# Kernel tuning notes

Hardware: AMD Instinct MI355X
Metric: run time of the kernel (lower is better)

Reference implementation:

```python
import jax, jax.numpy as jnp
import numpy as np

LEAKY = 0.2  # tf.nn.leaky_relu default alpha
E_SZ = [64, 64, 16]
F_SZ = [128, 128, 8]
N_MAPS, C, H, W = 64, 1, 32, 32
B = 8192


def _leaky(x):
    return jnp.where(x >= 0, x, LEAKY * x)


def func_theta(x, theta, sz, in_sz):
    # x: [B, in_sz]; theta: [B, total]; per-sample MLP with weights sliced from theta
    y = x
    offset = 0
    n = len(sz)
    for i, out_sz in enumerate(sz):
        w_sz = in_sz * out_sz
        Wm = theta[:, offset:offset + w_sz].reshape(-1, in_sz, out_sz)
        offset += w_sz
        b = theta[:, offset:offset + out_sz]
        offset += out_sz
        y = jnp.einsum('bi,bio->bo', y, Wm) + b
        if i < n - 1:
            y = _leaky(y)
        in_sz = out_sz
    return y


def setup_inputs() -> dict:
    key = jax.random.key(0)
    ks = jax.random.split(key, 16)

    def g(k, shape, scale):
        return (jax.random.normal(k, shape, dtype=jnp.float32) * scale)

    inp = {
        'indices': jax.random.randint(ks[0], (B,), 0, N_MAPS, dtype=jnp.int32),
        'states': jax.random.normal(ks[1], (B, 4), dtype=jnp.float32),
        'maps': jax.random.normal(ks[2], (N_MAPS, C, H, W), dtype=jnp.float32),
        'fc1_w': g(ks[3], (C * H * W, 256), 1.0 / np.sqrt(C * H * W)),
        'fc1_b': jnp.zeros((256,), jnp.float32),
        'fc2_w': g(ks[4], (256, 128), 1.0 / np.sqrt(256)),
        'fc2_b': jnp.zeros((128,), jnp.float32),
        'fc3_w': g(ks[5], (128, 128), 1.0 / np.sqrt(128)),
        'fc3_b': jnp.zeros((128,), jnp.float32),
        'bn_w': g(ks[6], (128, 32), 1.0 / np.sqrt(128)),
        'bn_b': jnp.zeros((32,), jnp.float32),
        'e_w': g(ks[7], (32, 5456), 1e-5),
        'e_b': g(ks[8], (5456,), 1e-3),
        'f_w': g(ks[9], (32, 21768), 1e-5),
        'f_b': g(ks[10], (21768,), 1e-3),
    }
    return inp


def reference(indices, states, maps, fc1_w, fc1_b, fc2_w, fc2_b, fc3_w, fc3_b,
              bn_w, bn_b, e_w, e_b, f_w, f_b):
    # gather maps per sample and flatten (NCHW -> NHWC transpose is a no-op after flatten
    # mathematically, but keep the exact data layout of the original)
    m = jnp.transpose(maps[indices], (0, 2, 3, 1)).astype(jnp.float32)  # [B,H,W,C]
    z = m.reshape(m.shape[0], -1)

    # hypernet trunk
    z = _leaky(z @ fc1_w + fc1_b)
    z = _leaky(z @ fc2_w + fc2_b)
    z = _leaky(z @ fc3_w + fc3_b)
    z = z @ bn_w + bn_b  # bottleneck, no activation
    theta_e = z @ e_w + e_b  # [B, 5456]
    theta_f = z @ f_w + f_b  # [B, 21768]

    S = states[:, 0:2]
    G = states[:, 2:4]
    e_s = func_theta(S, theta_e, E_SZ, 2)
    e_g = func_theta(G, theta_e, E_SZ, 2)
    zf = jnp.concatenate([e_s, e_g], axis=-1)  # [B, 32]
    ang = func_theta(zf, theta_f, F_SZ, 2 * E_SZ[-1])  # [B, 8]
    pts = jnp.concatenate([jnp.sin(ang), jnp.cos(ang)], axis=-1)  # [B, 16]
    return pts
```

## Files before the change

### kernel.cpp

```cpp
#include <hip/hip_runtime.h>
#include <hip/hip_bf16.h>


#define LEAKY 0.2f
#define NCLS 64
#define B_TOT 8192
#define NSLICE 4
#define ESTRIDE 68
#define FSTRIDE 132


__device__ __forceinline__ float lrelu(float x) { return x >= 0.f ? x : LEAKY * x; }

__global__ __launch_bounds__(1024) void backbone_bucket_kernel(
    const float* __restrict__ maps,
    const float* __restrict__ fc1_w, const float* __restrict__ fc1_b,
    const float* __restrict__ fc2_w, const float* __restrict__ fc2_b,
    const float* __restrict__ fc3_w, const float* __restrict__ fc3_b,
    const float* __restrict__ bn_w,  const float* __restrict__ bn_b,
    float* __restrict__ z,
    const int* __restrict__ idx, int* __restrict__ counts,
    int* __restrict__ offsets, int* __restrict__ perm)
{
    __shared__ float m[1024];
    __shared__ __align__(16) float4 red4[1024];
    __shared__ __align__(16) float h1[256];
    __shared__ __align__(16) float h2[128];
    __shared__ __align__(16) float h3[128];
    __shared__ int cnt[16][64];
    __shared__ int wcur[16][64];

    const int t = threadIdx.x;

    if (blockIdx.x == 64) {
        const int w = t >> 6;
        cnt[w][t & 63] = 0;
        __syncthreads();
        int my[8];
#pragma unroll
        for (int r = 0; r < 8; ++r) {
            my[r] = idx[r * 1024 + t];
            atomicAdd(&cnt[w][my[r]], 1);
        }
        __syncthreads();
        if (t < 64) {
            int run = 0;
#pragma unroll
            for (int w2 = 0; w2 < 16; ++w2) {
                const int v = cnt[w2][t];
                wcur[w2][t] = run;
                run += v;
            }
            counts[t] = run;
            int x = run;
            for (int d = 1; d < 64; d <<= 1) {
                const int y = __shfl_up(x, d, 64);
                if (t >= d) x += y;
            }
            const int basec = x - run;
            offsets[t] = basec;
#pragma unroll
            for (int w2 = 0; w2 < 16; ++w2) wcur[w2][t] += basec;
        }
        __syncthreads();
#pragma unroll
        for (int r = 0; r < 8; ++r) {
            const int p = atomicAdd(&wcur[w][my[r]], 1);
            perm[p] = r * 1024 + t;
        }
        return;
    }

    const int c = blockIdx.x;
    m[t] = maps[(size_t)c * 1024 + t];
    __syncthreads();

    {
        const int og = t & 63, ks = t >> 6;
        const float* wp = fc1_w + og * 4;
        float4 acc = {0.f, 0.f, 0.f, 0.f};
#pragma unroll 8
        for (int i = 0; i < 64; ++i) {
            const int k = ks * 64 + i;
            const float mk = m[k];
            const float4 w = *(const float4*)&wp[(size_t)k * 256];
            acc.x += mk * w.x; acc.y += mk * w.y;
            acc.z += mk * w.z; acc.w += mk * w.w;
        }
        red4[t] = acc;
    }
    __syncthreads();
    if (t < 64) {
        float4 a = *(const float4*)&fc1_b[t * 4];
#pragma unroll
        for (int r = 0; r < 16; ++r) {
            const float4 v = red4[r * 64 + t];
            a.x += v.x; a.y += v.y; a.z += v.z; a.w += v.w;
        }
        a.x = lrelu(a.x); a.y = lrelu(a.y); a.z = lrelu(a.z); a.w = lrelu(a.w);
        *(float4*)&h1[t * 4] = a;
    }
    __syncthreads();
    {
        const int og = t & 31, ks = t >> 5;
        float4 acc = {0.f, 0.f, 0.f, 0.f};
#pragma unroll
        for (int i = 0; i < 8; ++i) {
            const int k = ks * 8 + i;
            const float hk = h1[k];
            const float4 w = *(const float4*)&fc2_w[k * 128 + og * 4];
            acc.x += hk * w.x; acc.y += hk * w.y;
            acc.z += hk * w.z; acc.w += hk * w.w;
        }
        red4[t] = acc;
    }
    __syncthreads();
    if (t < 32) {
        float4 a = *(const float4*)&fc2_b[t * 4];
#pragma unroll
        for (int r = 0; r < 32; ++r) {
            const float4 v = red4[r * 32 + t];
            a.x += v.x; a.y += v.y; a.z += v.z; a.w += v.w;
        }
        a.x = lrelu(a.x); a.y = lrelu(a.y); a.z = lrelu(a.z); a.w = lrelu(a.w);
        *(float4*)&h2[t * 4] = a;
    }
    __syncthreads();
    {
        const int og = t & 31, ks = t >> 5;
        float4 acc = {0.f, 0.f, 0.f, 0.f};
#pragma unroll
        for (int i = 0; i < 4; ++i) {
            const int k = ks * 4 + i;
            const float hk = h2[k];
            const float4 w = *(const float4*)&fc3_w[k * 128 + og * 4];
            acc.x += hk * w.x; acc.y += hk * w.y;
            acc.z += hk * w.z; acc.w += hk * w.w;
        }
        red4[t] = acc;
    }
    __syncthreads();
    if (t < 32) {
        float4 a = *(const float4*)&fc3_b[t * 4];
#pragma unroll
        for (int r = 0; r < 32; ++r) {
            const float4 v = red4[r * 32 + t];
            a.x += v.x; a.y += v.y; a.z += v.z; a.w += v.w;
        }
        a.x = lrelu(a.x); a.y = lrelu(a.y); a.z = lrelu(a.z); a.w = lrelu(a.w);
        *(float4*)&h3[t * 4] = a;
    }
    __syncthreads();
    {
        const int og = t & 7, ks = t >> 3;
        const float hk = h3[ks];
        const float4 w = *(const float4*)&bn_w[ks * 32 + og * 4];
        float4 acc;
        acc.x = hk * w.x; acc.y = hk * w.y; acc.z = hk * w.z; acc.w = hk * w.w;
        red4[t] = acc;
    }
    __syncthreads();
    if (t < 8) {
        float4 a = *(const float4*)&bn_b[t * 4];
#pragma unroll
        for (int r = 0; r < 128; ++r) {
            const float4 v = red4[r * 8 + t];
            a.x += v.x; a.y += v.y; a.z += v.z; a.w += v.w;
        }
        *(float4*)&z[c * 32 + t * 4] = a;
    }
}

__global__ __launch_bounds__(256) void theta_kernel(
    const float* __restrict__ z,
    const float* __restrict__ e_w, const float* __restrict__ e_b,
    const float* __restrict__ f_w, const float* __restrict__ f_b,
    float* __restrict__ th_e, float* __restrict__ th_f)
{
    __shared__ __align__(16) float zl[2048];
    const int t = threadIdx.x;
    ((float4*)zl)[t]       = ((const float4*)z)[t];
    ((float4*)zl)[t + 256] = ((const float4*)z)[t + 256];
    __syncthreads();

    int j = blockIdx.x * 256 + t;
    const int cbase = blockIdx.y * 8;
    const float* wbase;
    float* op;
    int stride;
    float bias;
    if (j < 5456) {
        wbase = e_w + j; bias = e_b[j]; op = th_e + j; stride = 5456;
    } else {
        const int jj = j - 5456;
        if (jj >= 21768) return;
        wbase = f_w + jj; bias = f_b[jj]; op = th_f + jj; stride = 21768;
    }
    float wk[32];
#pragma unroll
    for (int k = 0; k < 32; ++k) wk[k] = wbase[(size_t)k * stride];

#pragma unroll
    for (int cc = 0; cc < 8; cc += 4) {
        const int c0 = cbase + cc;
        float a0 = bias, a1 = bias, a2 = bias, a3 = bias;
#pragma unroll
        for (int k4 = 0; k4 < 8; ++k4) {
            const float4 z0 = *(const float4*)&zl[(c0 + 0) * 32 + k4 * 4];
            const float4 z1 = *(const float4*)&zl[(c0 + 1) * 32 + k4 * 4];
            const float4 z2 = *(const float4*)&zl[(c0 + 2) * 32 + k4 * 4];
            const float4 z3 = *(const float4*)&zl[(c0 + 3) * 32 + k4 * 4];
            const float w0 = wk[k4 * 4], w1 = wk[k4 * 4 + 1];
            const float w2 = wk[k4 * 4 + 2], w3 = wk[k4 * 4 + 3];
            a0 += z0.x * w0 + z0.y * w1 + z0.z * w2 + z0.w * w3;
            a1 += z1.x * w0 + z1.y * w1 + z1.z * w2 + z1.w * w3;
            a2 += z2.x * w0 + z2.y * w1 + z2.z * w2 + z2.w * w3;
            a3 += z3.x * w0 + z3.y * w1 + z3.z * w2 + z3.w * w3;
        }
        op[(size_t)(c0 + 0) * stride] = a0;
        op[(size_t)(c0 + 1) * stride] = a1;
        op[(size_t)(c0 + 2) * stride] = a2;
        op[(size_t)(c0 + 3) * stride] = a3;
    }
}

__global__ __launch_bounds__(512) void func_kernel(
    const float* __restrict__ states,
    const float* __restrict__ th_e_all, const float* __restrict__ th_f_all,
    const int* __restrict__ counts, const int* __restrict__ offsets,
    const int* __restrict__ perm, float* __restrict__ out)
{
    __shared__ __align__(16) float wbuf[5392];
    __shared__ __align__(16) float w3fb[1160];
    __shared__ __align__(16) float actA[4352];
    __shared__ __align__(16) float actB[4352];
    __shared__ __align__(16) float part[512];

    const int c = blockIdx.x;
    const int s = blockIdx.y;
    const int nb   = counts[c];
    const int base = offsets[c];
    const int chunk = (nb + NSLICE - 1) / NSLICE;
    const int k0 = s * chunk;
    const int k1 = (nb < k0 + chunk) ? nb : (k0 + chunk);
    const int cnt = (k1 > k0) ? (k1 - k0) : 0;
    if (cnt == 0) return;

    const float* te = th_e_all + (size_t)c * 5456;
    const float* tf = th_f_all + (size_t)c * 21768;

    const int t   = threadIdx.x;
    const int vbs = t & 15;
    const int ce  = (t >> 4) * 2;
    const int fbs = t & 7;
    const int cf  = (t >> 3) * 2;

    for (int j = t * 4; j < 1160; j += 2048)
        *(float4*)&w3fb[j] = *(const float4*)&tf[20608 + j];
    for (int j = t * 4; j < 5392; j += 2048)
        *(float4*)&wbuf[j] = *(const float4*)&te[j];

    const int passes = (cnt + 31) >> 5;
    for (int p = 0; p < passes; ++p) {
        __syncthreads();
        if (p) {
            for (int j = t * 4; j < 5392; j += 2048)
                *(float4*)&wbuf[j] = *(const float4*)&te[j];
            __syncthreads();
        }

        const int kkA = k0 + p * 32 + vbs;
        const int kkB = kkA + 16;
        const int biA = (kkA < k1) ? perm[base + kkA] : 0;
        const int biB = (kkB < k1) ? perm[base + kkB] : 0;
        const float4 stA = *(const float4*)&states[(size_t)biA * 4];
        const float4 stB = *(const float4*)&states[(size_t)biB * 4];
        const float i0[4] = {stA.x, stB.x, stA.z, stB.z};
        const float i1[4] = {stA.y, stB.y, stA.w, stB.w};

        {
            const float2 wa = *(const float2*)&wbuf[ce];
            const float2 wb = *(const float2*)&wbuf[64 + ce];
            const float2 bb = *(const float2*)&wbuf[128 + ce];
#pragma unroll
            for (int j = 0; j < 4; ++j) {
                float2 o;
                o.x = lrelu(i0[j] * wa.x + i1[j] * wb.x + bb.x);
                o.y = lrelu(i0[j] * wa.y + i1[j] * wb.y + bb.y);
                *(float2*)&actA[(vbs + 16 * j) * ESTRIDE + ce] = o;
            }
        }
        __syncthreads();

        {
            float a0[4] = {0, 0, 0, 0}, a1[4] = {0, 0, 0, 0};
#pragma unroll 4
            for (int k4 = 0; k4 < 16; ++k4) {
                float4 y[4];
#pragma unroll
                for (int j = 0; j < 4; ++j)
                    y[j] = *(const float4*)&actA[(vbs + 16 * j) * ESTRIDE + k4 * 4];
#pragma unroll
                for (int u = 0; u < 4; ++u) {
                    const float2 w = *(const float2*)&wbuf[192 + (k4 * 4 + u) * 64 + ce];
#pragma unroll
                    for (int j = 0; j < 4; ++j) {
                        const float yv = (&y[j].x)[u];
                        a0[j] += yv * w.x;
                        a1[j] += yv * w.y;
                    }
                }
            }
            const float2 b2 = *(const float2*)&wbuf[4288 + ce];
#pragma unroll
            for (int j = 0; j < 4; ++j) {
                float2 o;
                o.x = lrelu(a0[j] + b2.x);
                o.y = lrelu(a1[j] + b2.y);
                *(float2*)&actB[(vbs + 16 * j) * ESTRIDE + ce] = o;
            }
        }
        __syncthreads();

        if (t < 256) {
            const int c3 = t >> 4;
            float a[4] = {0, 0, 0, 0};
#pragma unroll 4
            for (int k4 = 0; k4 < 16; ++k4) {
                float4 y[4];
#pragma unroll
                for (int j = 0; j < 4; ++j)
                    y[j] = *(const float4*)&actB[(vbs + 16 * j) * ESTRIDE + k4 * 4];
#pragma unroll
                for (int u = 0; u < 4; ++u) {
                    const float w = wbuf[4352 + (k4 * 4 + u) * 16 + c3];
#pragma unroll
                    for (int j = 0; j < 4; ++j) a[j] += (&y[j].x)[u] * w;
                }
            }
            const float b3 = wbuf[5376 + c3];
#pragma unroll
            for (int j = 0; j < 4; ++j) {
                const int vb = vbs + 16 * j;
                actA[(vb & 31) * FSTRIDE + (vb >> 5) * 16 + c3] = a[j] + b3;
            }
        }
        __syncthreads();

        for (int j = t * 4; j < 4224; j += 2048)
            *(float4*)&wbuf[j] = *(const float4*)&tf[j];
        __syncthreads();

        {
            float a0[4] = {0, 0, 0, 0}, a1[4] = {0, 0, 0, 0};
#pragma unroll
            for (int k4 = 0; k4 < 8; ++k4) {
                float4 y[4];
#pragma unroll
                for (int j = 0; j < 4; ++j)
                    y[j] = *(const float4*)&actA[(fbs + 8 * j) * FSTRIDE + k4 * 4];
#pragma unroll
                for (int u = 0; u < 4; ++u) {
                    const float2 w = *(const float2*)&wbuf[(k4 * 4 + u) * 128 + cf];
#pragma unroll
                    for (int j = 0; j < 4; ++j) {
                        const float yv = (&y[j].x)[u];
                        a0[j] += yv * w.x;
                        a1[j] += yv * w.y;
                    }
                }
            }
            const float2 b1 = *(const float2*)&wbuf[4096 + cf];
#pragma unroll
            for (int j = 0; j < 4; ++j) {
                float2 o;
                o.x = lrelu(a0[j] + b1.x);
                o.y = lrelu(a1[j] + b1.y);
                *(float2*)&actB[(fbs + 8 * j) * FSTRIDE + cf] = o;
            }
        }
        __syncthreads();

        {
            float a0[4] = {0, 0, 0, 0}, a1[4] = {0, 0, 0, 0};
#pragma unroll
            for (int h = 0; h < 4; ++h) {
                if (h) __syncthreads();
                for (int j = t * 4; j < 4096; j += 2048)
                    *(float4*)&wbuf[j] = *(const float4*)&tf[4224 + h * 4096 + j];
                __syncthreads();
#pragma unroll 4
                for (int k4 = 0; k4 < 8; ++k4) {
                    float4 y[4];
#pragma unroll
                    for (int j = 0; j < 4; ++j)
                        y[j] = *(const float4*)&actB[(fbs + 8 * j) * FSTRIDE + h * 32 + k4 * 4];
#pragma unroll
                    for (int u = 0; u < 4; ++u) {
                        const float2 w = *(const float2*)&wbuf[(k4 * 4 + u) * 128 + cf];
#pragma unroll
                        for (int j = 0; j < 4; ++j) {
                            const float yv = (&y[j].x)[u];
                            a0[j] += yv * w.x;
                            a1[j] += yv * w.y;
                        }
                    }
                }
            }
            const float2 b2 = *(const float2*)&w3fb[cf];
#pragma unroll
            for (int j = 0; j < 4; ++j) {
                float2 o;
                o.x = lrelu(a0[j] + b2.x);
                o.y = lrelu(a1[j] + b2.y);
                *(float2*)&actA[(fbs + 8 * j) * FSTRIDE + cf] = o;
            }
        }
        __syncthreads();

        {
            const int bat = t & 31, c8 = (t >> 5) & 7, kh = t >> 8;
            float a = 0.f;
#pragma unroll 4
            for (int k4 = kh * 16; k4 < kh * 16 + 16; ++k4) {
                const float4 y = *(const float4*)&actA[bat * FSTRIDE + k4 * 4];
#pragma unroll
                for (int u = 0; u < 4; ++u)
                    a += (&y.x)[u] * w3fb[128 + (k4 * 4 + u) * 8 + c8];
            }
            part[kh * 256 + bat * 8 + c8] = a;
        }
        __syncthreads();
        if (t < 256) {
            const int bat = t & 31, c8 = t >> 5;
            const int kk = k0 + p * 32 + bat;
            if (kk < k1) {
                const int bi = perm[base + kk];
                const float a = part[bat * 8 + c8] + part[256 + bat * 8 + c8]
                              + w3fb[1152 + c8];
                out[(size_t)bi * 16 + c8]     = __sinf(a);
                out[(size_t)bi * 16 + 8 + c8] = __cosf(a);
            }
        }
    }
}

extern "C" void kernel_launch(void* const* d_in, const int* in_sizes, int n_in,
                              void* d_out, int out_size, void* d_ws, size_t ws_size,
                              hipStream_t stream)
{
    const int*   indices = (const int*)  d_in[0];
    const float* states  = (const float*)d_in[1];
    const float* maps    = (const float*)d_in[2];
    const float* fc1_w   = (const float*)d_in[3];
    const float* fc1_b   = (const float*)d_in[4];
    const float* fc2_w   = (const float*)d_in[5];
    const float* fc2_b   = (const float*)d_in[6];
    const float* fc3_w   = (const float*)d_in[7];
    const float* fc3_b   = (const float*)d_in[8];
    const float* bn_w    = (const float*)d_in[9];
    const float* bn_b    = (const float*)d_in[10];
    const float* e_w     = (const float*)d_in[11];
    const float* e_b     = (const float*)d_in[12];
    const float* f_w     = (const float*)d_in[13];
    const float* f_b     = (const float*)d_in[14];
    float* out = (float*)d_out;

    float* ws   = (float*)d_ws;
    float* z    = ws;
    float* th_e = ws + 2048;
    float* th_f = ws + 351232;
    int* counts  = (int*)(ws + 1744384);
    int* offsets = counts + 64;
    int* perm    = counts + 128;

    backbone_bucket_kernel<<<65, 1024, 0, stream>>>(
        maps, fc1_w, fc1_b, fc2_w, fc2_b, fc3_w, fc3_b, bn_w, bn_b, z,
        indices, counts, offsets, perm);
    theta_kernel<<<dim3(107, 8), 256, 0, stream>>>(
        z, e_w, e_b, f_w, f_b, th_e, th_f);
    func_kernel<<<dim3(NCLS, NSLICE), 512, 0, stream>>>(
        states, th_e, th_f, counts, offsets, perm, out);
}
```

Measured before the change: 146.4 us.

## Halve per-pass batch, double slices, and prefetch theta weights into registers

The func kernel now processes 16 samples per pass instead of 32 and uses 8 slices per class instead of 4, so more blocks are launched. Each thread works on one sample with four output columns. Theta weight chunks are prefetched into registers one stage ahead, and stage-2 weights are loaded in two 8192-float halves rather than four, to overlap global loads with compute. Shared memory use drops and launch bounds request 4 blocks per CU for higher occupancy. The trade-off is more register pressure and redundant weight loads across the extra slices.

New measurement: 157.6 us. 7.7% more time.

```diff
diff --git a/kernel.cpp b/kernel.cpp
--- a/kernel.cpp
+++ b/kernel.cpp
@@ -5,9 +5,9 @@
 #define LEAKY 0.2f
 #define NCLS 64
 #define B_TOT 8192
-#define NSLICE 4
-#define ESTRIDE 68
-#define FSTRIDE 132
+#define NSLICE 8
+#define EST 68
+#define FST 132
 
 
 __device__ __forceinline__ float lrelu(float x) { return x >= 0.f ? x : LEAKY * x; }
@@ -224,16 +224,16 @@
     }
 }
 
-__global__ __launch_bounds__(512) void func_kernel(
+__global__ __launch_bounds__(512, 4) void func_kernel(
     const float* __restrict__ states,
     const float* __restrict__ th_e_all, const float* __restrict__ th_f_all,
     const int* __restrict__ counts, const int* __restrict__ offsets,
     const int* __restrict__ perm, float* __restrict__ out)
 {
-    __shared__ __align__(16) float wbuf[5392];
+    __shared__ __align__(16) float wbuf[8192];
     __shared__ __align__(16) float w3fb[1160];
-    __shared__ __align__(16) float actA[4352];
-    __shared__ __align__(16) float actB[4352];
+    __shared__ __align__(16) float actA[2176];
+    __shared__ __align__(16) float actB[2176];
     __shared__ __align__(16) float part[512];
 
     const int c = blockIdx.x;
@@ -243,203 +243,210 @@
     const int chunk = (nb + NSLICE - 1) / NSLICE;
     const int k0 = s * chunk;
     const int k1 = (nb < k0 + chunk) ? nb : (k0 + chunk);
-    const int cnt = (k1 > k0) ? (k1 - k0) : 0;
-    if (cnt == 0) return;
+    const int cntq = (k1 > k0) ? (k1 - k0) : 0;
+    if (cntq == 0) return;
 
     const float* te = th_e_all + (size_t)c * 5456;
     const float* tf = th_f_all + (size_t)c * 21768;
 
     const int t   = threadIdx.x;
-    const int vbs = t & 15;
-    const int ce  = (t >> 4) * 2;
-    const int fbs = t & 7;
-    const int cf  = (t >> 3) * 2;
-
-    for (int j = t * 4; j < 1160; j += 2048)
-        *(float4*)&w3fb[j] = *(const float4*)&tf[20608 + j];
-    for (int j = t * 4; j < 5392; j += 2048)
-        *(float4*)&wbuf[j] = *(const float4*)&te[j];
-
-    const int passes = (cnt + 31) >> 5;
+    const int vb  = t & 31;
+    const int ecq = (t >> 5) * 4;
+    const int c16 = t >> 5;
+    const int b_  = vb & 15;
+    const int sg  = vb >> 4;
+    const int fb  = t & 15;
+    const int fcq = (t >> 4) * 4;
+    const int fb3 = t & 15, c8 = (t >> 4) & 7, kq = t >> 7;
+
+    for (int i = 0; i < 3; ++i) {
+        const int j = t * 4 + i * 2048;
+        if (j < 5392) *(float4*)&wbuf[j] = *(const float4*)&te[j];
+    }
+    if (t * 4 < 1160) *(float4*)&w3fb[t * 4] = *(const float4*)&tf[20608 + t * 4];
+    float4 pfA[3];
+#pragma unroll
+    for (int i = 0; i < 3; ++i) {
+        const int j = t * 4 + i * 2048;
+        pfA[i] = (j < 4224) ? *(const float4*)&tf[j] : float4{0, 0, 0, 0};
+    }
+
+    const int passes = (cntq + 15) >> 4;
     for (int p = 0; p < passes; ++p) {
-        __syncthreads();
-        if (p) {
-            for (int j = t * 4; j < 5392; j += 2048)
-                *(float4*)&wbuf[j] = *(const float4*)&te[j];
-            __syncthreads();
-        }
-
-        const int kkA = k0 + p * 32 + vbs;
-        const int kkB = kkA + 16;
-        const int biA = (kkA < k1) ? perm[base + kkA] : 0;
-        const int biB = (kkB < k1) ? perm[base + kkB] : 0;
-        const float4 stA = *(const float4*)&states[(size_t)biA * 4];
-        const float4 stB = *(const float4*)&states[(size_t)biB * 4];
-        const float i0[4] = {stA.x, stB.x, stA.z, stB.z};
-        const float i1[4] = {stA.y, stB.y, stA.w, stB.w};
-
-        {
-            const float2 wa = *(const float2*)&wbuf[ce];
-            const float2 wb = *(const float2*)&wbuf[64 + ce];
-            const float2 bb = *(const float2*)&wbuf[128 + ce];
-#pragma unroll
-            for (int j = 0; j < 4; ++j) {
-                float2 o;
-                o.x = lrelu(i0[j] * wa.x + i1[j] * wb.x + bb.x);
-                o.y = lrelu(i0[j] * wa.y + i1[j] * wb.y + bb.y);
-                *(float2*)&actA[(vbs + 16 * j) * ESTRIDE + ce] = o;
-            }
-        }
-        __syncthreads();
-
-        {
-            float a0[4] = {0, 0, 0, 0}, a1[4] = {0, 0, 0, 0};
+        const int kk = k0 + p * 16 + b_;
+        const bool valid = kk < k1;
+        const int bi = valid ? perm[base + kk] : 0;
+        const float2 sv = *(const float2*)&states[(size_t)bi * 4 + 2 * sg];
+
+        __syncthreads();
+
+        {
+            const float4 wa = *(const float4*)&wbuf[ecq];
+            const float4 wb = *(const float4*)&wbuf[64 + ecq];
+            const float4 bb = *(const float4*)&wbuf[128 + ecq];
+            float4 o;
+            o.x = lrelu(sv.x * wa.x + sv.y * wb.x + bb.x);
+            o.y = lrelu(sv.x * wa.y + sv.y * wb.y + bb.y);
+            o.z = lrelu(sv.x * wa.z + sv.y * wb.z + bb.z);
+            o.w = lrelu(sv.x * wa.w + sv.y * wb.w + bb.w);
+            *(float4*)&actA[vb * EST + ecq] = o;
+        }
+        __syncthreads();
+
+        {
+            float4 acc = {0, 0, 0, 0};
 #pragma unroll 4
             for (int k4 = 0; k4 < 16; ++k4) {
-                float4 y[4];
-#pragma unroll
-                for (int j = 0; j < 4; ++j)
-                    y[j] = *(const float4*)&actA[(vbs + 16 * j) * ESTRIDE + k4 * 4];
+                const float4 y = *(const float4*)&actA[vb * EST + k4 * 4];
 #pragma unroll
                 for (int u = 0; u < 4; ++u) {
-                    const float2 w = *(const float2*)&wbuf[192 + (k4 * 4 + u) * 64 + ce];
-#pragma unroll
-                    for (int j = 0; j < 4; ++j) {
-                        const float yv = (&y[j].x)[u];
-                        a0[j] += yv * w.x;
-                        a1[j] += yv * w.y;
-                    }
+                    const float4 w = *(const float4*)&wbuf[192 + (k4 * 4 + u) * 64 + ecq];
+                    const float yv = (&y.x)[u];
+                    acc.x += yv * w.x; acc.y += yv * w.y;
+                    acc.z += yv * w.z; acc.w += yv * w.w;
                 }
             }
-            const float2 b2 = *(const float2*)&wbuf[4288 + ce];
-#pragma unroll
-            for (int j = 0; j < 4; ++j) {
-                float2 o;
-                o.x = lrelu(a0[j] + b2.x);
-                o.y = lrelu(a1[j] + b2.y);
-                *(float2*)&actB[(vbs + 16 * j) * ESTRIDE + ce] = o;
-            }
-        }
-        __syncthreads();
-
-        if (t < 256) {
-            const int c3 = t >> 4;
-            float a[4] = {0, 0, 0, 0};
+            const float4 bb = *(const float4*)&wbuf[4288 + ecq];
+            float4 o;
+            o.x = lrelu(acc.x + bb.x); o.y = lrelu(acc.y + bb.y);
+            o.z = lrelu(acc.z + bb.z); o.w = lrelu(acc.w + bb.w);
+            *(float4*)&actB[vb * EST + ecq] = o;
+        }
+        __syncthreads();
+
+        {
+            float a = 0.f;
 #pragma unroll 4
             for (int k4 = 0; k4 < 16; ++k4) {
-                float4 y[4];
-#pragma unroll
-                for (int j = 0; j < 4; ++j)
-                    y[j] = *(const float4*)&actB[(vbs + 16 * j) * ESTRIDE + k4 * 4];
+                const float4 y = *(const float4*)&actB[vb * EST + k4 * 4];
+#pragma unroll
+                for (int u = 0; u < 4; ++u)
+                    a += (&y.x)[u] * wbuf[4352 + (k4 * 4 + u) * 16 + c16];
+            }
+            a += wbuf[5376 + c16];
+            actA[b_ * FST + sg * 16 + c16] = a;
+        }
+        __syncthreads();
+
+        for (int i = 0; i < 3; ++i) {
+            const int j = t * 4 + i * 2048;
+            if (j < 4224) *(float4*)&wbuf[j] = pfA[i];
+        }
+        float4 pfH[4];
+#pragma unroll
+        for (int i = 0; i < 4; ++i)
+            pfH[i] = *(const float4*)&tf[4224 + t * 4 + i * 2048];
+        __syncthreads();
+
+        {
+            float4 acc = {0, 0, 0, 0};
+#pragma unroll
+            for (int k4 = 0; k4 < 8; ++k4) {
+                const float4 y = *(const float4*)&actA[fb * FST + k4 * 4];
 #pragma unroll
                 for (int u = 0; u < 4; ++u) {
-                    const float w = wbuf[4352 + (k4 * 4 + u) * 16 + c3];
-#pragma unroll
-                    for (int j = 0; j < 4; ++j) a[j] += (&y[j].x)[u] * w;
+                    const float4 w = *(const float4*)&wbuf[(k4 * 4 + u) * 128 + fcq];
+                    const float yv = (&y.x)[u];
+                    acc.x += yv * w.x; acc.y += yv * w.y;
+                    acc.z += yv * w.z; acc.w += yv * w.w;
                 }
             }
-            const float b3 = wbuf[5376 + c3];
-#pragma unroll
-            for (int j = 0; j < 4; ++j) {
-                const int vb = vbs + 16 * j;
-                actA[(vb & 31) * FSTRIDE + (vb >> 5) * 16 + c3] = a[j] + b3;
-            }
-        }
-        __syncthreads();
-
-        for (int j = t * 4; j < 4224; j += 2048)
-            *(float4*)&wbuf[j] = *(const float4*)&tf[j];
-        __syncthreads();
-
-        {
-            float a0[4] = {0, 0, 0, 0}, a1[4] = {0, 0, 0, 0};
-#pragma unroll
-            for (int k4 = 0; k4 < 8; ++k4) {
-                float4 y[4];
-#pragma unroll
-                for (int j = 0; j < 4; ++j)
-                    y[j] = *(const float4*)&actA[(fbs + 8 * j) * FSTRIDE + k4 * 4];
+            const float4 bb = *(const float4*)&wbuf[4096 + fcq];
+            float4 o;
+            o.x = lrelu(acc.x + bb.x); o.y = lrelu(acc.y + bb.y);
+            o.z = lrelu(acc.z + bb.z); o.w = lrelu(acc.w + bb.w);
+            *(float4*)&actB[fb * FST + fcq] = o;
+        }
+        __syncthreads();
+
+        for (int i = 0; i < 4; ++i)
+            *(float4*)&wbuf[t * 4 + i * 2048] = pfH[i];
+#pragma unroll
+        for (int i = 0; i < 4; ++i)
+            pfH[i] = *(const float4*)&tf[12416 + t * 4 + i * 2048];
+        __syncthreads();
+
+        float4 acc2 = {0, 0, 0, 0};
+#pragma unroll 4
+        for (int k4 = 0; k4 < 16; ++k4) {
+            const float4 y = *(const float4*)&actB[fb * FST + k4 * 4];
+#pragma unroll
+            for (int u = 0; u < 4; ++u) {
+                const float4 w = *(const float4*)&wbuf[(k4 * 4 + u) * 128 + fcq];
+                const float yv = (&y.x)[u];
+                acc2.x += yv * w.x; acc2.y += yv * w.y;
+                acc2.z += yv * w.z; acc2.w += yv * w.w;
+            }
+        }
+        __syncthreads();
+
+        for (int i = 0; i < 4; ++i)
+            *(float4*)&wbuf[t * 4 + i * 2048] = pfH[i];
+        const bool more = (p + 1 < passes);
+        float4 pfE[3];
+        if (more) {
+#pragma unroll
+            for (int i = 0; i < 3; ++i) {
+                const int j = t * 4 + i * 2048;
+                pfE[i] = (j < 5392) ? *(const float4*)&te[j] : float4{0, 0, 0, 0};
+            }
+        }
+        __syncthreads();
+
+        {
+#pragma unroll 4
+            for (int k4 = 0; k4 < 16; ++k4) {
+                const float4 y = *(const float4*)&actB[fb * FST + 64 + k4 * 4];
 #pragma unroll
                 for (int u = 0; u < 4; ++u) {
-                    const float2 w = *(const float2*)&wbuf[(k4 * 4 + u) * 128 + cf];
-#pragma unroll
-                    for (int j = 0; j < 4; ++j) {
-                        const float yv = (&y[j].x)[u];
-                        a0[j] += yv * w.x;
-                        a1[j] += yv * w.y;
-                    }
+                    const float4 w = *(const float4*)&wbuf[(k4 * 4 + u) * 128 + fcq];
+                    const float yv = (&y.x)[u];
+                    acc2.x += yv * w.x; acc2.y += yv * w.y;
+                    acc2.z += yv * w.z; acc2.w += yv * w.w;
                 }
             }
-            const float2 b1 = *(const float2*)&wbuf[4096 + cf];
-#pragma unroll
-            for (int j = 0; j < 4; ++j) {
-                float2 o;
-                o.x = lrelu(a0[j] + b1.x);
-                o.y = lrelu(a1[j] + b1.y);
-                *(float2*)&actB[(fbs + 8 * j) * FSTRIDE + cf] = o;
-            }
-        }
-        __syncthreads();
-
-        {
-            float a0[4] = {0, 0, 0, 0}, a1[4] = {0, 0, 0, 0};
-#pragma unroll
-            for (int h = 0; h < 4; ++h) {
-                if (h) __syncthreads();
-                for (int j = t * 4; j < 4096; j += 2048)
-                    *(float4*)&wbuf[j] = *(const float4*)&tf[4224 + h * 4096 + j];
-                __syncthreads();
-#pragma unroll 4
-                for (int k4 = 0; k4 < 8; ++k4) {
-                    float4 y[4];
-#pragma unroll
-                    for (int j = 0; j < 4; ++j)
-                        y[j] = *(const float4*)&actB[(fbs + 8 * j) * FSTRIDE + h * 32 + k4 * 4];
-#pragma unroll
-                    for (int u = 0; u < 4; ++u) {
-                        const float2 w = *(const float2*)&wbuf[(k4 * 4 + u) * 128 + cf];
-#pragma unroll
-                        for (int j = 0; j < 4; ++j) {
-                            const float yv = (&y[j].x)[u];
-                            a0[j] += yv * w.x;
-                            a1[j] += yv * w.y;
-                        }
-                    }
-                }
-            }
-            const float2 b2 = *(const float2*)&w3fb[cf];
-#pragma unroll
-            for (int j = 0; j < 4; ++j) {
-                float2 o;
-                o.x = lrelu(a0[j] + b2.x);
-                o.y = lrelu(a1[j] + b2.y);
-                *(float2*)&actA[(fbs + 8 * j) * FSTRIDE + cf] = o;
-            }
-        }
-        __syncthreads();
-
-        {
-            const int bat = t & 31, c8 = (t >> 5) & 7, kh = t >> 8;
+            const float4 bb = *(const float4*)&w3fb[fcq];
+            float4 o;
+            o.x = lrelu(acc2.x + bb.x); o.y = lrelu(acc2.y + bb.y);
+            o.z = lrelu(acc2.z + bb.z); o.w = lrelu(acc2.w + bb.w);
+            *(float4*)&actA[fb * FST + fcq] = o;
+        }
+        __syncthreads();
+
+        {
             float a = 0.f;
-#pragma unroll 4
-            for (int k4 = kh * 16; k4 < kh * 16 + 16; ++k4) {
-                const float4 y = *(const float4*)&actA[bat * FSTRIDE + k4 * 4];
+#pragma unroll
+            for (int k4 = kq * 8; k4 < kq * 8 + 8; ++k4) {
+                const float4 y = *(const float4*)&actA[fb3 * FST + k4 * 4];
 #pragma unroll
                 for (int u = 0; u < 4; ++u)
                     a += (&y.x)[u] * w3fb[128 + (k4 * 4 + u) * 8 + c8];
             }
-            part[kh * 256 + bat * 8 + c8] = a;
-        }
-        __syncthreads();
-        if (t < 256) {
-            const int bat = t & 31, c8 = t >> 5;
-            const int kk = k0 + p * 32 + bat;
-            if (kk < k1) {
-                const int bi = perm[base + kk];
-                const float a = part[bat * 8 + c8] + part[256 + bat * 8 + c8]
-                              + w3fb[1152 + c8];
-                out[(size_t)bi * 16 + c8]     = __sinf(a);
-                out[(size_t)bi * 16 + 8 + c8] = __cosf(a);
+            part[kq * 128 + fb3 * 8 + c8] = a;
+        }
+        if (more) {
+            for (int i = 0; i < 3; ++i) {
+                const int j = t * 4 + i * 2048;
+                if (j < 5392) *(float4*)&wbuf[j] = pfE[i];
+            }
+#pragma unroll
+            for (int i = 0; i < 3; ++i) {
+                const int j = t * 4 + i * 2048;
+                pfA[i] = (j < 4224) ? *(const float4*)&tf[j] : float4{0, 0, 0, 0};
+            }
+        }
+        __syncthreads();
+
+        if (t < 128) {
+            const int bb = t >> 3, cc8 = t & 7;
+            const int kk2 = k0 + p * 16 + bb;
+            if (kk2 < k1) {
+                const int bi2 = perm[base + kk2];
+                const float a = part[bb * 8 + cc8] + part[128 + bb * 8 + cc8]
+                              + part[256 + bb * 8 + cc8] + part[384 + bb * 8 + cc8]
+                              + w3fb[1152 + cc8];
+                out[(size_t)bi2 * 16 + cc8]     = __sinf(a);
+                out[(size_t)bi2 * 16 + 8 + cc8] = __cosf(a);
             }
         }
     }
```

## Split func_kernel into smaller 256-thread blocks with twice the slices per class

Applied to the files above, without the earlier changes.

The per-class func_kernel now launches 8 slices per class instead of 4, with 256-thread blocks processing 16 samples per pass instead of 32. Thread-to-output mappings for all layers are remapped to match, and the activation and partial buffers shrink, so more blocks can fit per CU. The aim is more parallelism across the GPU for a grid that was small (256 blocks). The cost is that each block reloads the per-class theta weights from global memory, so weight traffic per sample roughly doubles.

After: 149.7 us. 1.02x slower.

```diff
diff --git a/kernel.cpp b/kernel.cpp
--- a/kernel.cpp
+++ b/kernel.cpp
@@ -5,9 +5,9 @@
 #define LEAKY 0.2f
 #define NCLS 64
 #define B_TOT 8192
-#define NSLICE 4
-#define ESTRIDE 68
-#define FSTRIDE 132
+#define NSLICE 8
+#define EST 68
+#define FST 132
 
 
 __device__ __forceinline__ float lrelu(float x) { return x >= 0.f ? x : LEAKY * x; }
@@ -224,7 +224,7 @@
     }
 }
 
-__global__ __launch_bounds__(512) void func_kernel(
+__global__ __launch_bounds__(256, 3) void func_kernel(
     const float* __restrict__ states,
     const float* __restrict__ th_e_all, const float* __restrict__ th_f_all,
     const int* __restrict__ counts, const int* __restrict__ offsets,
@@ -232,9 +232,9 @@
 {
     __shared__ __align__(16) float wbuf[5392];
     __shared__ __align__(16) float w3fb[1160];
-    __shared__ __align__(16) float actA[4352];
-    __shared__ __align__(16) float actB[4352];
-    __shared__ __align__(16) float part[512];
+    __shared__ __align__(16) float actA[2176];
+    __shared__ __align__(16) float actB[2176];
+    __shared__ __align__(16) float part[256];
 
     const int c = blockIdx.x;
     const int s = blockIdx.y;
@@ -243,34 +243,39 @@
     const int chunk = (nb + NSLICE - 1) / NSLICE;
     const int k0 = s * chunk;
     const int k1 = (nb < k0 + chunk) ? nb : (k0 + chunk);
-    const int cnt = (k1 > k0) ? (k1 - k0) : 0;
-    if (cnt == 0) return;
+    const int cntq = (k1 > k0) ? (k1 - k0) : 0;
+    if (cntq == 0) return;
 
     const float* te = th_e_all + (size_t)c * 5456;
     const float* tf = th_f_all + (size_t)c * 21768;
 
     const int t   = threadIdx.x;
-    const int vbs = t & 15;
-    const int ce  = (t >> 4) * 2;
-    const int fbs = t & 7;
-    const int cf  = (t >> 3) * 2;
-
-    for (int j = t * 4; j < 1160; j += 2048)
+    const int vbs = t & 7;
+    const int ce  = (t >> 3) * 2;
+    const int vb3 = t & 31;
+    const int c3  = (t >> 5) * 2;
+    const int fbs = t & 3;
+    const int cf  = (t >> 2) * 2;
+    const int b3  = t & 15;
+    const int c8  = (t >> 4) & 7;
+    const int kh  = t >> 7;
+
+    for (int j = t * 4; j < 5392; j += 1024)
+        *(float4*)&wbuf[j] = *(const float4*)&te[j];
+    for (int j = t * 4; j < 1160; j += 1024)
         *(float4*)&w3fb[j] = *(const float4*)&tf[20608 + j];
-    for (int j = t * 4; j < 5392; j += 2048)
-        *(float4*)&wbuf[j] = *(const float4*)&te[j];
-
-    const int passes = (cnt + 31) >> 5;
+
+    const int passes = (cntq + 15) >> 4;
     for (int p = 0; p < passes; ++p) {
-        __syncthreads();
         if (p) {
-            for (int j = t * 4; j < 5392; j += 2048)
+            __syncthreads();
+            for (int j = t * 4; j < 5392; j += 1024)
                 *(float4*)&wbuf[j] = *(const float4*)&te[j];
-            __syncthreads();
-        }
-
-        const int kkA = k0 + p * 32 + vbs;
-        const int kkB = kkA + 16;
+        }
+        __syncthreads();
+
+        const int kkA = k0 + p * 16 + vbs;
+        const int kkB = kkA + 8;
         const int biA = (kkA < k1) ? perm[base + kkA] : 0;
         const int biB = (kkB < k1) ? perm[base + kkB] : 0;
         const float4 stA = *(const float4*)&states[(size_t)biA * 4];
@@ -287,7 +292,7 @@
                 float2 o;
                 o.x = lrelu(i0[j] * wa.x + i1[j] * wb.x + bb.x);
                 o.y = lrelu(i0[j] * wa.y + i1[j] * wb.y + bb.y);
-                *(float2*)&actA[(vbs + 16 * j) * ESTRIDE + ce] = o;
+                *(float2*)&actA[(vbs + 8 * j) * EST + ce] = o;
             }
         }
         __syncthreads();
@@ -299,7 +304,7 @@
                 float4 y[4];
 #pragma unroll
                 for (int j = 0; j < 4; ++j)
-                    y[j] = *(const float4*)&actA[(vbs + 16 * j) * ESTRIDE + k4 * 4];
+                    y[j] = *(const float4*)&actA[(vbs + 8 * j) * EST + k4 * 4];
 #pragma unroll
                 for (int u = 0; u < 4; ++u) {
                     const float2 w = *(const float2*)&wbuf[192 + (k4 * 4 + u) * 64 + ce];
@@ -317,37 +322,30 @@
                 float2 o;
                 o.x = lrelu(a0[j] + b2.x);
                 o.y = lrelu(a1[j] + b2.y);
-                *(float2*)&actB[(vbs + 16 * j) * ESTRIDE + ce] = o;
-            }
-        }
-        __syncthreads();
-
-        if (t < 256) {
-            const int c3 = t >> 4;
-            float a[4] = {0, 0, 0, 0};
+                *(float2*)&actB[(vbs + 8 * j) * EST + ce] = o;
+            }
+        }
+        __syncthreads();
+
+        {
+            float a0 = 0.f, a1 = 0.f;
 #pragma unroll 4
             for (int k4 = 0; k4 < 16; ++k4) {
-                float4 y[4];
-#pragma unroll
-                for (int j = 0; j < 4; ++j)
-                    y[j] = *(const float4*)&actB[(vbs + 16 * j) * ESTRIDE + k4 * 4];
+                const float4 y = *(const float4*)&actB[vb3 * EST + k4 * 4];
 #pragma unroll
                 for (int u = 0; u < 4; ++u) {
-                    const float w = wbuf[4352 + (k4 * 4 + u) * 16 + c3];
-#pragma unroll
-                    for (int j = 0; j < 4; ++j) a[j] += (&y[j].x)[u] * w;
+                    const int i = k4 * 4 + u;
+                    a0 += (&y.x)[u] * wbuf[4352 + i * 16 + c3];
+                    a1 += (&y.x)[u] * wbuf[4352 + i * 16 + c3 + 1];
                 }
             }
-            const float b3 = wbuf[5376 + c3];
-#pragma unroll
-            for (int j = 0; j < 4; ++j) {
-                const int vb = vbs + 16 * j;
-                actA[(vb & 31) * FSTRIDE + (vb >> 5) * 16 + c3] = a[j] + b3;
-            }
-        }
-        __syncthreads();
-
-        for (int j = t * 4; j < 4224; j += 2048)
+            const int fo = (vb3 & 15) * FST + (vb3 >> 4) * 16 + c3;
+            actA[fo]     = a0 + wbuf[5376 + c3];
+            actA[fo + 1] = a1 + wbuf[5376 + c3 + 1];
+        }
+        __syncthreads();
+
+        for (int j = t * 4; j < 4224; j += 1024)
             *(float4*)&wbuf[j] = *(const float4*)&tf[j];
         __syncthreads();
 
@@ -358,7 +356,7 @@
                 float4 y[4];
 #pragma unroll
                 for (int j = 0; j < 4; ++j)
-                    y[j] = *(const float4*)&actA[(fbs + 8 * j) * FSTRIDE + k4 * 4];
+                    y[j] = *(const float4*)&actA[(fbs + 4 * j) * FST + k4 * 4];
 #pragma unroll
                 for (int u = 0; u < 4; ++u) {
                     const float2 w = *(const float2*)&wbuf[(k4 * 4 + u) * 128 + cf];
@@ -376,7 +374,7 @@
                 float2 o;
                 o.x = lrelu(a0[j] + b1.x);
                 o.y = lrelu(a1[j] + b1.y);
-                *(float2*)&actB[(fbs + 8 * j) * FSTRIDE + cf] = o;
+                *(float2*)&actB[(fbs + 4 * j) * FST + cf] = o;
             }
         }
         __syncthreads();
@@ -385,8 +383,7 @@
             float a0[4] = {0, 0, 0, 0}, a1[4] = {0, 0, 0, 0};
 #pragma unroll
             for (int h = 0; h < 4; ++h) {
-                if (h) __syncthreads();
-                for (int j = t * 4; j < 4096; j += 2048)
+                for (int j = t * 4; j < 4096; j += 1024)
                     *(float4*)&wbuf[j] = *(const float4*)&tf[4224 + h * 4096 + j];
                 __syncthreads();
 #pragma unroll 4
@@ -394,7 +391,7 @@
                     float4 y[4];
 #pragma unroll
                     for (int j = 0; j < 4; ++j)
-                        y[j] = *(const float4*)&actB[(fbs + 8 * j) * FSTRIDE + h * 32 + k4 * 4];
+                        y[j] = *(const float4*)&actB[(fbs + 4 * j) * FST + h * 32 + k4 * 4];
 #pragma unroll
                     for (int u = 0; u < 4; ++u) {
                         const float2 w = *(const float2*)&wbuf[(k4 * 4 + u) * 128 + cf];
@@ -406,6 +403,7 @@
                         }
                     }
                 }
+                __syncthreads();
             }
             const float2 b2 = *(const float2*)&w3fb[cf];
 #pragma unroll
@@ -413,33 +411,33 @@
                 float2 o;
                 o.x = lrelu(a0[j] + b2.x);
                 o.y = lrelu(a1[j] + b2.y);
-                *(float2*)&actA[(fbs + 8 * j) * FSTRIDE + cf] = o;
-            }
-        }
-        __syncthreads();
-
-        {
-            const int bat = t & 31, c8 = (t >> 5) & 7, kh = t >> 8;
+                *(float2*)&actA[(fbs + 4 * j) * FST + cf] = o;
+            }
+        }
+        __syncthreads();
+
+        {
             float a = 0.f;
-#pragma unroll 4
+#pragma unroll
             for (int k4 = kh * 16; k4 < kh * 16 + 16; ++k4) {
-                const float4 y = *(const float4*)&actA[bat * FSTRIDE + k4 * 4];
+                const float4 y = *(const float4*)&actA[b3 * FST + k4 * 4];
 #pragma unroll
                 for (int u = 0; u < 4; ++u)
                     a += (&y.x)[u] * w3fb[128 + (k4 * 4 + u) * 8 + c8];
             }
-            part[kh * 256 + bat * 8 + c8] = a;
-        }
-        __syncthreads();
-        if (t < 256) {
-            const int bat = t & 31, c8 = t >> 5;
-            const int kk = k0 + p * 32 + bat;
-            if (kk < k1) {
-                const int bi = perm[base + kk];
-                const float a = part[bat * 8 + c8] + part[256 + bat * 8 + c8]
-                              + w3fb[1152 + c8];
-                out[(size_t)bi * 16 + c8]     = __sinf(a);
-                out[(size_t)bi * 16 + 8 + c8] = __cosf(a);
+            part[kh * 128 + b3 * 8 + c8] = a;
+        }
+        __syncthreads();
+
+        if (t < 128) {
+            const int bb = t >> 3, cc8 = t & 7;
+            const int kk2 = k0 + p * 16 + bb;
+            if (kk2 < k1) {
+                const int bi2 = perm[base + kk2];
+                const float a = part[bb * 8 + cc8] + part[128 + bb * 8 + cc8]
+                              + w3fb[1152 + cc8];
+                out[(size_t)bi2 * 16 + cc8]     = __sinf(a);
+                out[(size_t)bi2 * 16 + 8 + cc8] = __cosf(a);
             }
         }
     }
@@ -479,6 +477,6 @@
         indices, counts, offsets, perm);
     theta_kernel<<<dim3(107, 8), 256, 0, stream>>>(
         z, e_w, e_b, f_w, f_b, th_e, th_f);
-    func_kernel<<<dim3(NCLS, NSLICE), 512, 0, stream>>>(
+    func_kernel<<<dim3(NCLS, NSLICE), 256, 0, stream>>>(
         states, th_e, th_f, counts, offsets, perm, out);
 }
```
